# Kernel tuning notes

Measured on AMD Instinct MI355X. Metric: run time of the kernel, lower is better.

The kernel has to match this reference:

```python
import jax, jax.numpy as jnp
import numpy as np

N_NODES = 100000
N_EDGES = 1600000
IN_DIM, HID_DIM, OUT_DIM = 32, 64, 8


def sage_conv(x, src, dst, W_l, b_l, W_r, n_nodes):
    # PyG SAGEConv (aggr='mean', root_weight=True):
    # out_i = W_l @ mean_{j in N(i)} x_j + b_l + W_r @ x_i
    msg_sum = jax.ops.segment_sum(x[src], dst, num_segments=n_nodes)  # [N, F]
    deg = jax.ops.segment_sum(jnp.ones((src.shape[0],), x.dtype), dst,
                              num_segments=n_nodes)  # [N]
    agg = msg_sum / jnp.maximum(deg, 1.0)[:, None]
    return agg @ W_l.T + b_l + x @ W_r.T


def setup_inputs() -> dict:
    key = jax.random.key(0)
    ks = jax.random.split(key, 8)
    x = jax.random.normal(ks[0], (N_NODES, IN_DIM), dtype=jnp.float32)
    edge_index = jax.random.randint(ks[1], (2, N_EDGES), 0, N_NODES, dtype=jnp.int64)
    s1 = 1.0 / np.sqrt(IN_DIM)
    s2 = 1.0 / np.sqrt(HID_DIM)
    return {
        "x": x,
        "edge_index": edge_index,
        "W1_l": jax.random.uniform(ks[2], (HID_DIM, IN_DIM), jnp.float32, -s1, s1),
        "b1": jnp.zeros((HID_DIM,), jnp.float32),
        "W1_r": jax.random.uniform(ks[3], (HID_DIM, IN_DIM), jnp.float32, -s1, s1),
        "W2_l": jax.random.uniform(ks[4], (OUT_DIM, HID_DIM), jnp.float32, -s2, s2),
        "b2": jnp.zeros((OUT_DIM,), jnp.float32),
        "W2_r": jax.random.uniform(ks[5], (OUT_DIM, HID_DIM), jnp.float32, -s2, s2),
    }


def reference(x, edge_index, W1_l, b1, W1_r, W2_l, b2, W2_r):
    src, dst = edge_index[0], edge_index[1]
    h = sage_conv(x, src, dst, W1_l, b1, W1_r, N_NODES)
    h = jax.nn.relu(h)
    out = sage_conv(h, src, dst, W2_l, b2, W2_r, N_NODES)
    return out
```

## Files before the change

kernel.cpp:

```cpp
#include <hip/hip_runtime.h>

#define N_NODES 100000
#define N_EDGES 1600000
#define IN_DIM 32
#define HID_DIM 64
#define OUT_DIM 8
#define CAP 64
#define CHUNK 4096
#define NCHUNK ((N_EDGES + CHUNK - 1) / CHUNK)
#define SLICE_W (N_NODES / 8)
#define QCAP 262144
#define BBLK 2048

typedef unsigned short u16;
typedef unsigned int u32;
typedef unsigned long long ull;

__device__ __forceinline__ float bf2f(u16 v) {
    return __uint_as_float(((u32)v) << 16);
}

__device__ __forceinline__ u16 f2bf(float f) {
    u32 u = __float_as_uint(f);
    u32 lsb = (u >> 16) & 1u;
    u += 0x7fffu + lsb;
    return (u16)(u >> 16);
}

__device__ __forceinline__ float ldf(const void* p, size_t i, int bf) {
    return bf ? bf2f(((const u16*)p)[i]) : ((const float*)p)[i];
}

__global__ __launch_bounds__(256) void k_part(
    const int* __restrict__ ei, const u32* __restrict__ xw,
    const void* __restrict__ W1l, const void* __restrict__ b1,
    const void* __restrict__ W1r,
    const void* __restrict__ W2l, const void* __restrict__ b2,
    const void* __restrict__ W2r,
    int* __restrict__ qcnt, u32* __restrict__ qbuf,
    int* __restrict__ cnt,
    float* __restrict__ tW1l, float* __restrict__ tW1r,
    float* __restrict__ tW2l, float* __restrict__ tW2r,
    float* __restrict__ tb1, float* __restrict__ tb2)
{
    __shared__ int shv, bfv;
    __shared__ int hist[4][8], wbase[4][8], lcur[4][8], gbase[8];
    int t = threadIdx.x, w = t >> 6;
    if (t < 64) {
        int v = ei[2 * t + 1];
        ull m1 = __ballot(v == 0);
        u32 wd = xw[t];
        u32 b = (wd >> 8) & 0x7fu;
        ull m2 = __ballot(b >= 0x38u && b <= 0x41u);
        if (t == 0) {
            shv = (m1 == ~0ULL) ? 1 : 0;
            bfv = (__popcll(m2) >= 56) ? 1 : 0;
        }
    }
    if (t < 32) { hist[t >> 3][t & 7] = 0; lcur[t >> 3][t & 7] = 0; }
    __syncthreads();
    int sh = shv, bf = bfv;

    for (int i = blockIdx.x * 256 + t; i < N_NODES; i += NCHUNK * 256) cnt[i] = 0;

    if (blockIdx.x < 16) {
        for (int i = blockIdx.x * 256 + t; i < HID_DIM * IN_DIM; i += 16 * 256) {
            int o = i / IN_DIM, k = i % IN_DIM;
            tW1l[k * HID_DIM + o] = ldf(W1l, i, bf);
            tW1r[k * HID_DIM + o] = ldf(W1r, i, bf);
        }
        for (int i = blockIdx.x * 256 + t; i < OUT_DIM * HID_DIM; i += 16 * 256) {
            int o = i / HID_DIM, k = i % HID_DIM;
            tW2l[k * OUT_DIM + o] = ldf(W2l, i, bf);
            tW2r[k * OUT_DIM + o] = ldf(W2r, i, bf);
        }
        if (blockIdx.x == 0) {
            if (t < HID_DIM) tb1[t] = ldf(b1, t, bf);
            if (t < OUT_DIM) tb2[t] = ldf(b2, t, bf);
        }
    }

    int e0 = blockIdx.x * CHUNK;
    int myd[16], mys[16];
    #pragma unroll
    for (int i = 0; i < 16; i++) {
        int e = e0 + i * 256 + t;
        if (e < N_EDGES) {
            size_t off = (size_t)e << sh;
            mys[i] = ei[off];
            int d = ei[((size_t)N_EDGES << sh) + off];
            myd[i] = d;
            atomicAdd(&hist[w][d / SLICE_W], 1);
        } else myd[i] = -1;
    }
    __syncthreads();
    if (t < 8) {
        int tot = hist[0][t] + hist[1][t] + hist[2][t] + hist[3][t];
        gbase[t] = atomicAdd(&qcnt[t], tot);
    }
    __syncthreads();
    if (t < 32) {
        int w2 = t >> 3, s = t & 7;
        int p = gbase[s];
        for (int w3 = 0; w3 < w2; w3++) p += hist[w3][s];
        wbase[w2][s] = p;
    }
    __syncthreads();
    #pragma unroll
    for (int i = 0; i < 16; i++) {
        int d = myd[i];
        if (d >= 0) {
            int s = d / SLICE_W;
            int p = wbase[w][s] + atomicAdd(&lcur[w][s], 1);
            qbuf[(size_t)s * QCAP + p] = ((u32)mys[i] << 14) | (u32)(d - s * SLICE_W);
        }
    }
}

__global__ __launch_bounds__(256) void k_build2(
    const int* __restrict__ qcnt, const u32* __restrict__ qbuf,
    int* __restrict__ cnt, int* __restrict__ slot)
{
    int slice = blockIdx.x & 7, bi = blockIdx.x >> 3;
    int m = qcnt[slice];
    int lo = slice * SLICE_W;
    const u32* q = qbuf + (size_t)slice * QCAP;
    for (int i = bi * 256 + threadIdx.x; i < m; i += (BBLK / 8) * 256) {
        u32 u = q[i];
        int d = lo + (int)(u & 0x3FFFu);
        int s = (int)(u >> 14);
        int pos = atomicAdd(&cnt[d], 1);
        if (pos < CAP) slot[(size_t)d * CAP + pos] = s;
    }
}

__global__ __launch_bounds__(256, 8) void k_sage1(
    const void* __restrict__ x, const int* __restrict__ cnt,
    const int* __restrict__ slot,
    const float* __restrict__ tW1l, const float* __restrict__ tW1r,
    const float* __restrict__ tW2l, const float* __restrict__ tW2r,
    const float* __restrict__ tb1, const float* __restrict__ tb2,
    const int* __restrict__ flags_unused,
    u16* __restrict__ gbuf, float* __restrict__ rbuf,
    const u32* __restrict__ xw)
{
    __shared__ float aggbuf[8][IN_DIM];
    __shared__ float xbuf[8][IN_DIM];
    __shared__ float hbuf[8][HID_DIM + 1];
    __shared__ int bfv;

    int t = threadIdx.x;
    if (t < 64) {
        u32 wd = xw[t];
        u32 b = (wd >> 8) & 0x7fu;
        ull m2 = __ballot(b >= 0x38u && b <= 0x41u);
        if (t == 0) bfv = (__popcll(m2) >= 56) ? 1 : 0;
    }
    __syncthreads();
    int bf = bfv;
    int wid = t >> 6, lane = t & 63;
    int half = lane >> 5;
    int g2 = (lane >> 3) & 3;
    int l = lane & 7;
    int ns = wid * 2 + half;
    int n = blockIdx.x * 8 + ns;
    int deg = cnt[n];
    int cl = (deg < CAP) ? deg : CAP;
    const int* srow = slot + (size_t)n * CAP;

    float a0 = 0, a1 = 0, a2 = 0, a3 = 0;
    float c0 = 0, c1 = 0, c2 = 0, c3 = 0;
    float d0 = 0, d1 = 0, d2 = 0, d3 = 0;
    float e0 = 0, e1 = 0, e2 = 0, e3 = 0;
    int j = g2;
    for (; j + 12 < cl; j += 16) {
        int sA = srow[j];
        int sB = srow[j + 4];
        int sC = srow[j + 8];
        int sD = srow[j + 12];
        if (bf) {
            ushort4 vA = reinterpret_cast<const ushort4*>((const u16*)x + (size_t)sA * IN_DIM)[l];
            ushort4 vB = reinterpret_cast<const ushort4*>((const u16*)x + (size_t)sB * IN_DIM)[l];
            ushort4 vC = reinterpret_cast<const ushort4*>((const u16*)x + (size_t)sC * IN_DIM)[l];
            ushort4 vD = reinterpret_cast<const ushort4*>((const u16*)x + (size_t)sD * IN_DIM)[l];
            a0 += bf2f(vA.x); a1 += bf2f(vA.y); a2 += bf2f(vA.z); a3 += bf2f(vA.w);
            c0 += bf2f(vB.x); c1 += bf2f(vB.y); c2 += bf2f(vB.z); c3 += bf2f(vB.w);
            d0 += bf2f(vC.x); d1 += bf2f(vC.y); d2 += bf2f(vC.z); d3 += bf2f(vC.w);
            e0 += bf2f(vD.x); e1 += bf2f(vD.y); e2 += bf2f(vD.z); e3 += bf2f(vD.w);
        } else {
            float4 vA = reinterpret_cast<const float4*>((const float*)x + (size_t)sA * IN_DIM)[l];
            float4 vB = reinterpret_cast<const float4*>((const float*)x + (size_t)sB * IN_DIM)[l];
            float4 vC = reinterpret_cast<const float4*>((const float*)x + (size_t)sC * IN_DIM)[l];
            float4 vD = reinterpret_cast<const float4*>((const float*)x + (size_t)sD * IN_DIM)[l];
            a0 += vA.x; a1 += vA.y; a2 += vA.z; a3 += vA.w;
            c0 += vB.x; c1 += vB.y; c2 += vB.z; c3 += vB.w;
            d0 += vC.x; d1 += vC.y; d2 += vC.z; d3 += vC.w;
            e0 += vD.x; e1 += vD.y; e2 += vD.z; e3 += vD.w;
        }
    }
    for (; j + 4 < cl; j += 8) {
        int sA = srow[j];
        int sB = srow[j + 4];
        if (bf) {
            ushort4 vA = reinterpret_cast<const ushort4*>((const u16*)x + (size_t)sA * IN_DIM)[l];
            ushort4 vB = reinterpret_cast<const ushort4*>((const u16*)x + (size_t)sB * IN_DIM)[l];
            a0 += bf2f(vA.x); a1 += bf2f(vA.y); a2 += bf2f(vA.z); a3 += bf2f(vA.w);
            c0 += bf2f(vB.x); c1 += bf2f(vB.y); c2 += bf2f(vB.z); c3 += bf2f(vB.w);
        } else {
            float4 vA = reinterpret_cast<const float4*>((const float*)x + (size_t)sA * IN_DIM)[l];
            float4 vB = reinterpret_cast<const float4*>((const float*)x + (size_t)sB * IN_DIM)[l];
            a0 += vA.x; a1 += vA.y; a2 += vA.z; a3 += vA.w;
            c0 += vB.x; c1 += vB.y; c2 += vB.z; c3 += vB.w;
        }
    }
    if (j < cl) {
        int s = srow[j];
        if (bf) {
            ushort4 v = reinterpret_cast<const ushort4*>((const u16*)x + (size_t)s * IN_DIM)[l];
            a0 += bf2f(v.x); a1 += bf2f(v.y); a2 += bf2f(v.z); a3 += bf2f(v.w);
        } else {
            float4 v = reinterpret_cast<const float4*>((const float*)x + (size_t)s * IN_DIM)[l];
            a0 += v.x; a1 += v.y; a2 += v.z; a3 += v.w;
        }
    }
    a0 += c0 + d0 + e0;
    a1 += c1 + d1 + e1;
    a2 += c2 + d2 + e2;
    a3 += c3 + d3 + e3;
    a0 += __shfl_xor(a0, 8, 64);  a0 += __shfl_xor(a0, 16, 64);
    a1 += __shfl_xor(a1, 8, 64);  a1 += __shfl_xor(a1, 16, 64);
    a2 += __shfl_xor(a2, 8, 64);  a2 += __shfl_xor(a2, 16, 64);
    a3 += __shfl_xor(a3, 8, 64);  a3 += __shfl_xor(a3, 16, 64);
    if (g2 == 0) {
        aggbuf[ns][4 * l + 0] = a0; aggbuf[ns][4 * l + 1] = a1;
        aggbuf[ns][4 * l + 2] = a2; aggbuf[ns][4 * l + 3] = a3;
    } else if (g2 == 1) {
        float f0, f1, f2, f3;
        if (bf) {
            ushort4 v = reinterpret_cast<const ushort4*>((const u16*)x + (size_t)n * IN_DIM)[l];
            f0 = bf2f(v.x); f1 = bf2f(v.y); f2 = bf2f(v.z); f3 = bf2f(v.w);
        } else {
            float4 v = reinterpret_cast<const float4*>((const float*)x + (size_t)n * IN_DIM)[l];
            f0 = v.x; f1 = v.y; f2 = v.z; f3 = v.w;
        }
        xbuf[ns][4 * l + 0] = f0; xbuf[ns][4 * l + 1] = f1;
        xbuf[ns][4 * l + 2] = f2; xbuf[ns][4 * l + 3] = f3;
    }
    __syncthreads();

    float rd0 = 1.0f / fmaxf((float)__shfl(deg, 0, 64), 1.0f);
    float rd1 = 1.0f / fmaxf((float)__shfl(deg, 32, 64), 1.0f);
    int s0 = wid * 2, s1 = wid * 2 + 1;
    int o = lane;
    float bb = tb1[o];
    float acc0 = bb, acc1 = bb;
    #pragma unroll 8
    for (int k = 0; k < IN_DIM; k++) {
        float wl = tW1l[k * HID_DIM + o];
        float wr = tW1r[k * HID_DIM + o];
        acc0 += (aggbuf[s0][k] * rd0) * wl + xbuf[s0][k] * wr;
        acc1 += (aggbuf[s1][k] * rd1) * wl + xbuf[s1][k] * wr;
    }
    hbuf[s0][o] = fmaxf(acc0, 0.0f);
    hbuf[s1][o] = fmaxf(acc1, 0.0f);
    __syncthreads();

    float ga = 0.0f, ra = 0.0f;
    #pragma unroll 4
    for (int m = 0; m < 16; m++) {
        int k = g2 * 16 + m;
        float hv = hbuf[ns][k];
        ga += hv * tW2l[k * OUT_DIM + l];
        ra += hv * tW2r[k * OUT_DIM + l];
    }
    ga += __shfl_xor(ga, 8, 64);  ga += __shfl_xor(ga, 16, 64);
    ra += __shfl_xor(ra, 8, 64);  ra += __shfl_xor(ra, 16, 64);
    if (g2 == 0) {
        gbuf[(size_t)n * OUT_DIM + l] = f2bf(ga);
        rbuf[(size_t)n * OUT_DIM + l] = ra + tb2[l];
    }
}

__global__ __launch_bounds__(256) void k_sage3(
    const u16* __restrict__ gbuf, const float* __restrict__ rbuf,
    const int* __restrict__ cnt, const int* __restrict__ slot,
    const u32* __restrict__ xw, void* __restrict__ out)
{
    __shared__ int bfv;
    int t = threadIdx.x;
    if (t < 64) {
        u32 w = xw[t];
        u32 b = (w >> 8) & 0x7fu;
        ull m2 = __ballot(b >= 0x38u && b <= 0x41u);
        if (t == 0) bfv = (__popcll(m2) >= 56) ? 1 : 0;
    }
    __syncthreads();
    int grp = t >> 3, l = t & 7;
    int n = blockIdx.x * 32 + grp;
    int deg = cnt[n];
    int cl = (deg < CAP) ? deg : CAP;
    const int* srow = slot + (size_t)n * CAP;
    float a0 = 0.0f, a1 = 0.0f, a2 = 0.0f, a3 = 0.0f;
    int j = 0;
    for (; j + 3 < cl; j += 4) {
        int v0 = srow[j];
        int v1 = srow[j + 1];
        int v2 = srow[j + 2];
        int v3 = srow[j + 3];
        a0 += bf2f(gbuf[(size_t)v0 * OUT_DIM + l]);
        a1 += bf2f(gbuf[(size_t)v1 * OUT_DIM + l]);
        a2 += bf2f(gbuf[(size_t)v2 * OUT_DIM + l]);
        a3 += bf2f(gbuf[(size_t)v3 * OUT_DIM + l]);
    }
    for (; j < cl; j++) a0 += bf2f(gbuf[(size_t)srow[j] * OUT_DIM + l]);
    float res = (a0 + a1 + a2 + a3) / fmaxf((float)deg, 1.0f)
              + rbuf[(size_t)n * OUT_DIM + l];
    size_t oi = (size_t)n * OUT_DIM + l;
    if (bfv) ((u16*)out)[oi] = f2bf(res);
    else     ((float*)out)[oi] = res;
}

extern "C" void kernel_launch(void* const* d_in, const int* in_sizes, int n_in,
                              void* d_out, int out_size, void* d_ws, size_t ws_size,
                              hipStream_t stream) {
    const void* x   = d_in[0];
    const int*  ei  = (const int*)d_in[1];
    const void* W1l = d_in[2];
    const void* b1  = d_in[3];
    const void* W1r = d_in[4];
    const void* W2l = d_in[5];
    const void* b2  = d_in[6];
    const void* W2r = d_in[7];

    int* qcnt    = (int*)d_ws;
    int* cnt     = qcnt + 8;
    float* tW1l  = (float*)(cnt + N_NODES);
    float* tW1r  = tW1l + IN_DIM * HID_DIM;
    float* tW2l  = tW1r + IN_DIM * HID_DIM;
    float* tW2r  = tW2l + HID_DIM * OUT_DIM;
    float* tb1   = tW2r + HID_DIM * OUT_DIM;
    float* tb2   = tb1 + HID_DIM;
    int* slot    = (int*)(tb2 + OUT_DIM);
    u32* qbuf    = (u32*)(slot + (size_t)N_NODES * CAP);
    u16* gbuf    = (u16*)(qbuf + (size_t)8 * QCAP);
    float* rbuf  = (float*)(gbuf + (size_t)N_NODES * OUT_DIM);

    hipMemsetAsync(d_ws, 0, 8 * sizeof(int), stream);

    k_part<<<NCHUNK, 256, 0, stream>>>(ei, (const u32*)x,
                                       W1l, b1, W1r, W2l, b2, W2r,
                                       qcnt, qbuf, cnt,
                                       tW1l, tW1r, tW2l, tW2r, tb1, tb2);
    k_build2<<<BBLK, 256, 0, stream>>>(qcnt, qbuf, cnt, slot);
    k_sage1<<<N_NODES / 8, 256, 0, stream>>>(x, cnt, slot, tW1l, tW1r,
                                             tW2l, tW2r, tb1, tb2, nullptr,
                                             gbuf, rbuf, (const u32*)x);
    k_sage3<<<N_NODES / 32, 256, 0, stream>>>(gbuf, rbuf, cnt, slot,
                                              (const u32*)x, d_out);
}
```

Measured before the change: 254.0 us.

## Replace CSR slot build with 128-node bucket queues and LDS atomic aggregation

Partitions edges into 782 buckets of 128 destination nodes and drops the per-node slot table and the build kernel. Each layer kernel now processes one bucket per block, accumulating neighbor features into shared memory with atomics and computing degrees locally. This removes one kernel launch and the global cnt/slot scatter traffic. In exchange it adds heavy LDS atomic contention, silently truncates any bucket past 2560 edges, and leaves only 782 blocks of parallelism.

Measured after the change: 585.8 us. +130.6%, slower.

```diff
diff --git a/kernel.cpp b/kernel.cpp
--- a/kernel.cpp
+++ b/kernel.cpp
@@ -5,12 +5,11 @@
 #define IN_DIM 32
 #define HID_DIM 64
 #define OUT_DIM 8
-#define CAP 64
+#define BK 128
+#define NBKT ((N_NODES + BK - 1) / BK)
+#define QC 2560
 #define CHUNK 4096
 #define NCHUNK ((N_EDGES + CHUNK - 1) / CHUNK)
-#define SLICE_W (N_NODES / 8)
-#define QCAP 262144
-#define BBLK 2048
 
 typedef unsigned short u16;
 typedef unsigned int u32;
@@ -31,21 +30,32 @@
     return bf ? bf2f(((const u16*)p)[i]) : ((const float*)p)[i];
 }
 
-__global__ __launch_bounds__(256) void k_part(
+__device__ __forceinline__ void acc8(float* ar, int k0, uint4 r) {
+    atomicAdd(&ar[k0 + 0], bf2f((u16)r.x)); atomicAdd(&ar[k0 + 1], bf2f((u16)(r.x >> 16)));
+    atomicAdd(&ar[k0 + 2], bf2f((u16)r.y)); atomicAdd(&ar[k0 + 3], bf2f((u16)(r.y >> 16)));
+    atomicAdd(&ar[k0 + 4], bf2f((u16)r.z)); atomicAdd(&ar[k0 + 5], bf2f((u16)(r.z >> 16)));
+    atomicAdd(&ar[k0 + 6], bf2f((u16)r.w)); atomicAdd(&ar[k0 + 7], bf2f((u16)(r.w >> 16)));
+}
+
+__device__ __forceinline__ void acc4(float* ar, int k0, float4 v) {
+    atomicAdd(&ar[k0 + 0], v.x); atomicAdd(&ar[k0 + 1], v.y);
+    atomicAdd(&ar[k0 + 2], v.z); atomicAdd(&ar[k0 + 3], v.w);
+}
+
+__global__ __launch_bounds__(256) void k_part2(
     const int* __restrict__ ei, const u32* __restrict__ xw,
     const void* __restrict__ W1l, const void* __restrict__ b1,
     const void* __restrict__ W1r,
     const void* __restrict__ W2l, const void* __restrict__ b2,
     const void* __restrict__ W2r,
     int* __restrict__ qcnt, u32* __restrict__ qbuf,
-    int* __restrict__ cnt,
     float* __restrict__ tW1l, float* __restrict__ tW1r,
     float* __restrict__ tW2l, float* __restrict__ tW2r,
     float* __restrict__ tb1, float* __restrict__ tb2)
 {
     __shared__ int shv, bfv;
-    __shared__ int hist[4][8], wbase[4][8], lcur[4][8], gbase[8];
-    int t = threadIdx.x, w = t >> 6;
+    __shared__ int hist[NBKT], gbase[NBKT], lcur[NBKT];
+    int t = threadIdx.x;
     if (t < 64) {
         int v = ei[2 * t + 1];
         ull m1 = __ballot(v == 0);
@@ -57,11 +67,9 @@
             bfv = (__popcll(m2) >= 56) ? 1 : 0;
         }
     }
-    if (t < 32) { hist[t >> 3][t & 7] = 0; lcur[t >> 3][t & 7] = 0; }
+    for (int i = t; i < NBKT; i += 256) { hist[i] = 0; lcur[i] = 0; }
     __syncthreads();
     int sh = shv, bf = bfv;
-
-    for (int i = blockIdx.x * 256 + t; i < N_NODES; i += NCHUNK * 256) cnt[i] = 0;
 
     if (blockIdx.x < 16) {
         for (int i = blockIdx.x * 256 + t; i < HID_DIM * IN_DIM; i += 16 * 256) {
@@ -90,63 +98,40 @@
             mys[i] = ei[off];
             int d = ei[((size_t)N_EDGES << sh) + off];
             myd[i] = d;
-            atomicAdd(&hist[w][d / SLICE_W], 1);
+            atomicAdd(&hist[d >> 7], 1);
         } else myd[i] = -1;
     }
     __syncthreads();
-    if (t < 8) {
-        int tot = hist[0][t] + hist[1][t] + hist[2][t] + hist[3][t];
-        gbase[t] = atomicAdd(&qcnt[t], tot);
-    }
-    __syncthreads();
-    if (t < 32) {
-        int w2 = t >> 3, s = t & 7;
-        int p = gbase[s];
-        for (int w3 = 0; w3 < w2; w3++) p += hist[w3][s];
-        wbase[w2][s] = p;
+    for (int i = t; i < NBKT; i += 256) {
+        int h = hist[i];
+        gbase[i] = h ? atomicAdd(&qcnt[i], h) : 0;
     }
     __syncthreads();
     #pragma unroll
     for (int i = 0; i < 16; i++) {
         int d = myd[i];
         if (d >= 0) {
-            int s = d / SLICE_W;
-            int p = wbase[w][s] + atomicAdd(&lcur[w][s], 1);
-            qbuf[(size_t)s * QCAP + p] = ((u32)mys[i] << 14) | (u32)(d - s * SLICE_W);
-        }
-    }
-}
-
-__global__ __launch_bounds__(256) void k_build2(
+            int bk = d >> 7;
+            int p = gbase[bk] + atomicAdd(&lcur[bk], 1);
+            if (p < QC)
+                qbuf[(size_t)bk * QC + p] = ((u32)mys[i] << 7) | (u32)(d & 127);
+        }
+    }
+}
+
+__global__ __launch_bounds__(256, 4) void k_l1(
+    const void* __restrict__ x,
     const int* __restrict__ qcnt, const u32* __restrict__ qbuf,
-    int* __restrict__ cnt, int* __restrict__ slot)
-{
-    int slice = blockIdx.x & 7, bi = blockIdx.x >> 3;
-    int m = qcnt[slice];
-    int lo = slice * SLICE_W;
-    const u32* q = qbuf + (size_t)slice * QCAP;
-    for (int i = bi * 256 + threadIdx.x; i < m; i += (BBLK / 8) * 256) {
-        u32 u = q[i];
-        int d = lo + (int)(u & 0x3FFFu);
-        int s = (int)(u >> 14);
-        int pos = atomicAdd(&cnt[d], 1);
-        if (pos < CAP) slot[(size_t)d * CAP + pos] = s;
-    }
-}
-
-__global__ __launch_bounds__(256, 8) void k_sage1(
-    const void* __restrict__ x, const int* __restrict__ cnt,
-    const int* __restrict__ slot,
     const float* __restrict__ tW1l, const float* __restrict__ tW1r,
     const float* __restrict__ tW2l, const float* __restrict__ tW2r,
     const float* __restrict__ tb1, const float* __restrict__ tb2,
-    const int* __restrict__ flags_unused,
     u16* __restrict__ gbuf, float* __restrict__ rbuf,
     const u32* __restrict__ xw)
 {
-    __shared__ float aggbuf[8][IN_DIM];
-    __shared__ float xbuf[8][IN_DIM];
-    __shared__ float hbuf[8][HID_DIM + 1];
+    __shared__ float agg[BK][IN_DIM + 1];
+    __shared__ float xs[BK][IN_DIM];
+    __shared__ float hb[8][HID_DIM + 1];
+    __shared__ int degi[BK];
     __shared__ int bfv;
 
     int t = threadIdx.x;
@@ -156,136 +141,114 @@
         ull m2 = __ballot(b >= 0x38u && b <= 0x41u);
         if (t == 0) bfv = (__popcll(m2) >= 56) ? 1 : 0;
     }
+    for (int i = t; i < BK * (IN_DIM + 1); i += 256) ((float*)agg)[i] = 0.0f;
+    for (int i = t; i < BK; i += 256) degi[i] = 0;
     __syncthreads();
     int bf = bfv;
+    int b = blockIdx.x, nb = b * BK;
+
+    if (bf) {
+        const u32* xr = (const u32*)x + (size_t)nb * (IN_DIM / 2);
+        for (int i = t; i < BK * (IN_DIM / 2); i += 256) {
+            int r = i >> 4, c = i & 15;
+            u32 w = (nb + r < N_NODES) ? xr[i] : 0u;
+            xs[r][2 * c]     = bf2f((u16)w);
+            xs[r][2 * c + 1] = bf2f((u16)(w >> 16));
+        }
+    } else {
+        const float* xr = (const float*)x + (size_t)nb * IN_DIM;
+        for (int i = t; i < BK * IN_DIM; i += 256) {
+            xs[i >> 5][i & 31] = (nb + (i >> 5) < N_NODES) ? xr[i] : 0.0f;
+        }
+    }
+
+    int m = qcnt[b]; if (m > QC) m = QC;
+    const u32* q = qbuf + (size_t)b * QC;
+    if (bf) {
+        int i = t;
+        for (; i + 256 < m; i += 512) {
+            u32 uA = __builtin_nontemporal_load(&q[i]);
+            u32 uB = __builtin_nontemporal_load(&q[i + 256]);
+            int dA = uA & 127, sA = (int)(uA >> 7);
+            int dB = uB & 127, sB = (int)(uB >> 7);
+            const uint4* rA = (const uint4*)((const u16*)x + (size_t)sA * IN_DIM);
+            const uint4* rB = (const uint4*)((const u16*)x + (size_t)sB * IN_DIM);
+            uint4 a0 = rA[0], a1 = rA[1], a2 = rA[2], a3 = rA[3];
+            uint4 b0 = rB[0], b1_ = rB[1], b2_ = rB[2], b3 = rB[3];
+            atomicAdd(&degi[dA], 1); atomicAdd(&degi[dB], 1);
+            float* arA = agg[dA];
+            acc8(arA, 0, a0); acc8(arA, 8, a1); acc8(arA, 16, a2); acc8(arA, 24, a3);
+            float* arB = agg[dB];
+            acc8(arB, 0, b0); acc8(arB, 8, b1_); acc8(arB, 16, b2_); acc8(arB, 24, b3);
+        }
+        if (i < m) {
+            u32 u = __builtin_nontemporal_load(&q[i]);
+            int d7 = u & 127, s = (int)(u >> 7);
+            const uint4* r = (const uint4*)((const u16*)x + (size_t)s * IN_DIM);
+            uint4 a0 = r[0], a1 = r[1], a2 = r[2], a3 = r[3];
+            atomicAdd(&degi[d7], 1);
+            float* ar = agg[d7];
+            acc8(ar, 0, a0); acc8(ar, 8, a1); acc8(ar, 16, a2); acc8(ar, 24, a3);
+        }
+    } else {
+        for (int i = t; i < m; i += 256) {
+            u32 u = __builtin_nontemporal_load(&q[i]);
+            int d7 = u & 127, s = (int)(u >> 7);
+            const float4* r = (const float4*)((const float*)x + (size_t)s * IN_DIM);
+            float4 v0 = r[0], v1 = r[1], v2 = r[2], v3 = r[3];
+            float4 v4 = r[4], v5 = r[5], v6 = r[6], v7 = r[7];
+            atomicAdd(&degi[d7], 1);
+            float* ar = agg[d7];
+            acc4(ar, 0, v0);  acc4(ar, 4, v1);  acc4(ar, 8, v2);  acc4(ar, 12, v3);
+            acc4(ar, 16, v4); acc4(ar, 20, v5); acc4(ar, 24, v6); acc4(ar, 28, v7);
+        }
+    }
+    __syncthreads();
+
     int wid = t >> 6, lane = t & 63;
-    int half = lane >> 5;
-    int g2 = (lane >> 3) & 3;
-    int l = lane & 7;
-    int ns = wid * 2 + half;
-    int n = blockIdx.x * 8 + ns;
-    int deg = cnt[n];
-    int cl = (deg < CAP) ? deg : CAP;
-    const int* srow = slot + (size_t)n * CAP;
-
-    float a0 = 0, a1 = 0, a2 = 0, a3 = 0;
-    float c0 = 0, c1 = 0, c2 = 0, c3 = 0;
-    float d0 = 0, d1 = 0, d2 = 0, d3 = 0;
-    float e0 = 0, e1 = 0, e2 = 0, e3 = 0;
-    int j = g2;
-    for (; j + 12 < cl; j += 16) {
-        int sA = srow[j];
-        int sB = srow[j + 4];
-        int sC = srow[j + 8];
-        int sD = srow[j + 12];
-        if (bf) {
-            ushort4 vA = reinterpret_cast<const ushort4*>((const u16*)x + (size_t)sA * IN_DIM)[l];
-            ushort4 vB = reinterpret_cast<const ushort4*>((const u16*)x + (size_t)sB * IN_DIM)[l];
-            ushort4 vC = reinterpret_cast<const ushort4*>((const u16*)x + (size_t)sC * IN_DIM)[l];
-            ushort4 vD = reinterpret_cast<const ushort4*>((const u16*)x + (size_t)sD * IN_DIM)[l];
-            a0 += bf2f(vA.x); a1 += bf2f(vA.y); a2 += bf2f(vA.z); a3 += bf2f(vA.w);
-            c0 += bf2f(vB.x); c1 += bf2f(vB.y); c2 += bf2f(vB.z); c3 += bf2f(vB.w);
-            d0 += bf2f(vC.x); d1 += bf2f(vC.y); d2 += bf2f(vC.z); d3 += bf2f(vC.w);
-            e0 += bf2f(vD.x); e1 += bf2f(vD.y); e2 += bf2f(vD.z); e3 += bf2f(vD.w);
-        } else {
-            float4 vA = reinterpret_cast<const float4*>((const float*)x + (size_t)sA * IN_DIM)[l];
-            float4 vB = reinterpret_cast<const float4*>((const float*)x + (size_t)sB * IN_DIM)[l];
-            float4 vC = reinterpret_cast<const float4*>((const float*)x + (size_t)sC * IN_DIM)[l];
-            float4 vD = reinterpret_cast<const float4*>((const float*)x + (size_t)sD * IN_DIM)[l];
-            a0 += vA.x; a1 += vA.y; a2 += vA.z; a3 += vA.w;
-            c0 += vB.x; c1 += vB.y; c2 += vB.z; c3 += vB.w;
-            d0 += vC.x; d1 += vC.y; d2 += vC.z; d3 += vC.w;
-            e0 += vD.x; e1 += vD.y; e2 += vD.z; e3 += vD.w;
-        }
-    }
-    for (; j + 4 < cl; j += 8) {
-        int sA = srow[j];
-        int sB = srow[j + 4];
-        if (bf) {
-            ushort4 vA = reinterpret_cast<const ushort4*>((const u16*)x + (size_t)sA * IN_DIM)[l];
-            ushort4 vB = reinterpret_cast<const ushort4*>((const u16*)x + (size_t)sB * IN_DIM)[l];
-            a0 += bf2f(vA.x); a1 += bf2f(vA.y); a2 += bf2f(vA.z); a3 += bf2f(vA.w);
-            c0 += bf2f(vB.x); c1 += bf2f(vB.y); c2 += bf2f(vB.z); c3 += bf2f(vB.w);
-        } else {
-            float4 vA = reinterpret_cast<const float4*>((const float*)x + (size_t)sA * IN_DIM)[l];
-            float4 vB = reinterpret_cast<const float4*>((const float*)x + (size_t)sB * IN_DIM)[l];
-            a0 += vA.x; a1 += vA.y; a2 += vA.z; a3 += vA.w;
-            c0 += vB.x; c1 += vB.y; c2 += vB.z; c3 += vB.w;
-        }
-    }
-    if (j < cl) {
-        int s = srow[j];
-        if (bf) {
-            ushort4 v = reinterpret_cast<const ushort4*>((const u16*)x + (size_t)s * IN_DIM)[l];
-            a0 += bf2f(v.x); a1 += bf2f(v.y); a2 += bf2f(v.z); a3 += bf2f(v.w);
-        } else {
-            float4 v = reinterpret_cast<const float4*>((const float*)x + (size_t)s * IN_DIM)[l];
-            a0 += v.x; a1 += v.y; a2 += v.z; a3 += v.w;
-        }
-    }
-    a0 += c0 + d0 + e0;
-    a1 += c1 + d1 + e1;
-    a2 += c2 + d2 + e2;
-    a3 += c3 + d3 + e3;
-    a0 += __shfl_xor(a0, 8, 64);  a0 += __shfl_xor(a0, 16, 64);
-    a1 += __shfl_xor(a1, 8, 64);  a1 += __shfl_xor(a1, 16, 64);
-    a2 += __shfl_xor(a2, 8, 64);  a2 += __shfl_xor(a2, 16, 64);
-    a3 += __shfl_xor(a3, 8, 64);  a3 += __shfl_xor(a3, 16, 64);
-    if (g2 == 0) {
-        aggbuf[ns][4 * l + 0] = a0; aggbuf[ns][4 * l + 1] = a1;
-        aggbuf[ns][4 * l + 2] = a2; aggbuf[ns][4 * l + 3] = a3;
-    } else if (g2 == 1) {
-        float f0, f1, f2, f3;
-        if (bf) {
-            ushort4 v = reinterpret_cast<const ushort4*>((const u16*)x + (size_t)n * IN_DIM)[l];
-            f0 = bf2f(v.x); f1 = bf2f(v.y); f2 = bf2f(v.z); f3 = bf2f(v.w);
-        } else {
-            float4 v = reinterpret_cast<const float4*>((const float*)x + (size_t)n * IN_DIM)[l];
-            f0 = v.x; f1 = v.y; f2 = v.z; f3 = v.w;
-        }
-        xbuf[ns][4 * l + 0] = f0; xbuf[ns][4 * l + 1] = f1;
-        xbuf[ns][4 * l + 2] = f2; xbuf[ns][4 * l + 3] = f3;
-    }
-    __syncthreads();
-
-    float rd0 = 1.0f / fmaxf((float)__shfl(deg, 0, 64), 1.0f);
-    float rd1 = 1.0f / fmaxf((float)__shfl(deg, 32, 64), 1.0f);
-    int s0 = wid * 2, s1 = wid * 2 + 1;
     int o = lane;
     float bb = tb1[o];
-    float acc0 = bb, acc1 = bb;
-    #pragma unroll 8
-    for (int k = 0; k < IN_DIM; k++) {
-        float wl = tW1l[k * HID_DIM + o];
-        float wr = tW1r[k * HID_DIM + o];
-        acc0 += (aggbuf[s0][k] * rd0) * wl + xbuf[s0][k] * wr;
-        acc1 += (aggbuf[s1][k] * rd1) * wl + xbuf[s1][k] * wr;
-    }
-    hbuf[s0][o] = fmaxf(acc0, 0.0f);
-    hbuf[s1][o] = fmaxf(acc1, 0.0f);
-    __syncthreads();
-
-    float ga = 0.0f, ra = 0.0f;
-    #pragma unroll 4
-    for (int m = 0; m < 16; m++) {
-        int k = g2 * 16 + m;
-        float hv = hbuf[ns][k];
-        ga += hv * tW2l[k * OUT_DIM + l];
-        ra += hv * tW2r[k * OUT_DIM + l];
-    }
-    ga += __shfl_xor(ga, 8, 64);  ga += __shfl_xor(ga, 16, 64);
-    ra += __shfl_xor(ra, 8, 64);  ra += __shfl_xor(ra, 16, 64);
-    if (g2 == 0) {
-        gbuf[(size_t)n * OUT_DIM + l] = f2bf(ga);
-        rbuf[(size_t)n * OUT_DIM + l] = ra + tb2[l];
-    }
-}
-
-__global__ __launch_bounds__(256) void k_sage3(
+    int half = lane >> 5, g2 = (lane >> 3) & 3, l = lane & 7;
+    for (int pr = 0; pr < 16; pr++) {
+        int s0 = pr * 8 + wid * 2, s1 = s0 + 1;
+        float rd0 = 1.0f / fmaxf((float)degi[s0], 1.0f);
+        float rd1 = 1.0f / fmaxf((float)degi[s1], 1.0f);
+        float acc0 = bb, acc1 = bb;
+        #pragma unroll 8
+        for (int k = 0; k < IN_DIM; k++) {
+            float wl = tW1l[k * HID_DIM + o];
+            float wr = tW1r[k * HID_DIM + o];
+            acc0 += (agg[s0][k] * rd0) * wl + xs[s0][k] * wr;
+            acc1 += (agg[s1][k] * rd1) * wl + xs[s1][k] * wr;
+        }
+        hb[wid * 2][o]     = fmaxf(acc0, 0.0f);
+        hb[wid * 2 + 1][o] = fmaxf(acc1, 0.0f);
+        int hs = wid * 2 + half;
+        float ga = 0.0f, ra = 0.0f;
+        #pragma unroll 4
+        for (int mm = 0; mm < 16; mm++) {
+            int k = g2 * 16 + mm;
+            float hv = hb[hs][k];
+            ga += hv * tW2l[k * OUT_DIM + l];
+            ra += hv * tW2r[k * OUT_DIM + l];
+        }
+        ga += __shfl_xor(ga, 8, 64);  ga += __shfl_xor(ga, 16, 64);
+        ra += __shfl_xor(ra, 8, 64);  ra += __shfl_xor(ra, 16, 64);
+        int n = nb + s0 + half;
+        if (g2 == 0 && n < N_NODES) {
+            __builtin_nontemporal_store(f2bf(ga), &gbuf[(size_t)n * OUT_DIM + l]);
+            __builtin_nontemporal_store(ra + tb2[l], &rbuf[(size_t)n * OUT_DIM + l]);
+        }
+    }
+}
+
+__global__ __launch_bounds__(256) void k_l2(
     const u16* __restrict__ gbuf, const float* __restrict__ rbuf,
-    const int* __restrict__ cnt, const int* __restrict__ slot,
+    const int* __restrict__ qcnt, const u32* __restrict__ qbuf,
     const u32* __restrict__ xw, void* __restrict__ out)
 {
+    __shared__ float ag[BK][OUT_DIM + 1];
+    __shared__ int degi[BK];
     __shared__ int bfv;
     int t = threadIdx.x;
     if (t < 64) {
@@ -294,30 +257,43 @@
         ull m2 = __ballot(b >= 0x38u && b <= 0x41u);
         if (t == 0) bfv = (__popcll(m2) >= 56) ? 1 : 0;
     }
-    __syncthreads();
-    int grp = t >> 3, l = t & 7;
-    int n = blockIdx.x * 32 + grp;
-    int deg = cnt[n];
-    int cl = (deg < CAP) ? deg : CAP;
-    const int* srow = slot + (size_t)n * CAP;
-    float a0 = 0.0f, a1 = 0.0f, a2 = 0.0f, a3 = 0.0f;
-    int j = 0;
-    for (; j + 3 < cl; j += 4) {
-        int v0 = srow[j];
-        int v1 = srow[j + 1];
-        int v2 = srow[j + 2];
-        int v3 = srow[j + 3];
-        a0 += bf2f(gbuf[(size_t)v0 * OUT_DIM + l]);
-        a1 += bf2f(gbuf[(size_t)v1 * OUT_DIM + l]);
-        a2 += bf2f(gbuf[(size_t)v2 * OUT_DIM + l]);
-        a3 += bf2f(gbuf[(size_t)v3 * OUT_DIM + l]);
-    }
-    for (; j < cl; j++) a0 += bf2f(gbuf[(size_t)srow[j] * OUT_DIM + l]);
-    float res = (a0 + a1 + a2 + a3) / fmaxf((float)deg, 1.0f)
-              + rbuf[(size_t)n * OUT_DIM + l];
-    size_t oi = (size_t)n * OUT_DIM + l;
-    if (bfv) ((u16*)out)[oi] = f2bf(res);
-    else     ((float*)out)[oi] = res;
+    for (int i = t; i < BK * (OUT_DIM + 1); i += 256) ((float*)ag)[i] = 0.0f;
+    for (int i = t; i < BK; i += 256) degi[i] = 0;
+    __syncthreads();
+    int b = blockIdx.x, nb = b * BK;
+    int m = qcnt[b]; if (m > QC) m = QC;
+    const u32* q = qbuf + (size_t)b * QC;
+    int i = t;
+    for (; i + 256 < m; i += 512) {
+        u32 uA = __builtin_nontemporal_load(&q[i]);
+        u32 uB = __builtin_nontemporal_load(&q[i + 256]);
+        int dA = uA & 127, sA = (int)(uA >> 7);
+        int dB = uB & 127, sB = (int)(uB >> 7);
+        uint4 rA = *(const uint4*)(gbuf + (size_t)sA * OUT_DIM);
+        uint4 rB = *(const uint4*)(gbuf + (size_t)sB * OUT_DIM);
+        atomicAdd(&degi[dA], 1); atomicAdd(&degi[dB], 1);
+        acc8(ag[dA], 0, rA);
+        acc8(ag[dB], 0, rB);
+    }
+    if (i < m) {
+        u32 u = __builtin_nontemporal_load(&q[i]);
+        int d7 = u & 127, s = (int)(u >> 7);
+        uint4 r = *(const uint4*)(gbuf + (size_t)s * OUT_DIM);
+        atomicAdd(&degi[d7], 1);
+        acc8(ag[d7], 0, r);
+    }
+    __syncthreads();
+    for (int idx = t; idx < BK * OUT_DIM; idx += 256) {
+        int r = idx >> 3, l = idx & 7;
+        int n = nb + r;
+        if (n < N_NODES) {
+            float res = ag[r][l] / fmaxf((float)degi[r], 1.0f)
+                      + rbuf[(size_t)n * OUT_DIM + l];
+            size_t oi = (size_t)n * OUT_DIM + l;
+            if (bfv) ((u16*)out)[oi] = f2bf(res);
+            else     ((float*)out)[oi] = res;
+        }
+    }
 }
 
 extern "C" void kernel_launch(void* const* d_in, const int* in_sizes, int n_in,
@@ -333,28 +309,25 @@
     const void* W2r = d_in[7];
 
     int* qcnt    = (int*)d_ws;
-    int* cnt     = qcnt + 8;
-    float* tW1l  = (float*)(cnt + N_NODES);
+    float* tW1l  = (float*)(qcnt + 1024);
     float* tW1r  = tW1l + IN_DIM * HID_DIM;
     float* tW2l  = tW1r + IN_DIM * HID_DIM;
     float* tW2r  = tW2l + HID_DIM * OUT_DIM;
     float* tb1   = tW2r + HID_DIM * OUT_DIM;
     float* tb2   = tb1 + HID_DIM;
-    int* slot    = (int*)(tb2 + OUT_DIM);
-    u32* qbuf    = (u32*)(slot + (size_t)N_NODES * CAP);
-    u16* gbuf    = (u16*)(qbuf + (size_t)8 * QCAP);
+    u32* qbuf    = (u32*)(tb2 + OUT_DIM);
+    u16* gbuf    = (u16*)(qbuf + (size_t)NBKT * QC);
     float* rbuf  = (float*)(gbuf + (size_t)N_NODES * OUT_DIM);
 
-    hipMemsetAsync(d_ws, 0, 8 * sizeof(int), stream);
-
-    k_part<<<NCHUNK, 256, 0, stream>>>(ei, (const u32*)x,
-                                       W1l, b1, W1r, W2l, b2, W2r,
-                                       qcnt, qbuf, cnt,
-                                       tW1l, tW1r, tW2l, tW2r, tb1, tb2);
-    k_build2<<<BBLK, 256, 0, stream>>>(qcnt, qbuf, cnt, slot);
-    k_sage1<<<N_NODES / 8, 256, 0, stream>>>(x, cnt, slot, tW1l, tW1r,
-                                             tW2l, tW2r, tb1, tb2, nullptr,
-                                             gbuf, rbuf, (const u32*)x);
-    k_sage3<<<N_NODES / 32, 256, 0, stream>>>(gbuf, rbuf, cnt, slot,
-                                              (const u32*)x, d_out);
-}
+    hipMemsetAsync(d_ws, 0, 1024 * sizeof(int), stream);
+
+    k_part2<<<NCHUNK, 256, 0, stream>>>(ei, (const u32*)x,
+                                        W1l, b1, W1r, W2l, b2, W2r,
+                                        qcnt, qbuf,
+                                        tW1l, tW1r, tW2l, tW2r, tb1, tb2);
+    k_l1<<<NBKT, 256, 0, stream>>>(x, qcnt, qbuf,
+                                   tW1l, tW1r, tW2l, tW2r, tb1, tb2,
+                                   gbuf, rbuf, (const u32*)x);
+    k_l2<<<NBKT, 256, 0, stream>>>(gbuf, rbuf, qcnt, qbuf,
+                                   (const u32*)x, d_out);
+}
```
